# Kernel tuning notes

Hardware: AMD Instinct MI355X
Metric: run time of the kernel (lower is better)

The kernel has to match this reference:

```python
import jax, jax.numpy as jnp
import numpy as np

BS, T, NE, NA, ED = 32, 64, 32, 8, 128
H, A, NH, NACT = 512, 512, 8, 32
HD = A // NH  # 64
SCALE = np.float32(np.sqrt(HD))


def setup_inputs() -> dict:
    key = jax.random.key(0)
    ks = jax.random.split(key, 12)
    inputs = jax.random.normal(ks[0], (BS, T, NE, ED), jnp.float32)
    obs_mask = jax.random.randint(ks[1], (BS, T, NE, NE), 0, 2, jnp.int32)
    scenario_mask = jax.random.randint(ks[2], (BS, T, NE), 0, 2, jnp.int32)
    hidden_state = jnp.zeros((BS * NA, H), jnp.float32)
    g = lambda k, shp: jax.random.normal(k, shp, jnp.float32) * 0.05
    return {
        'inputs': inputs, 'obs_mask': obs_mask, 'scenario_mask': scenario_mask,
        'hidden_state': hidden_state,
        'W1': g(ks[3], (ED, H)), 'b1': jnp.zeros((H,), jnp.float32),
        'Wq': g(ks[4], (H, A)), 'bq': jnp.zeros((A,), jnp.float32),
        'Wk': g(ks[5], (H, A)), 'bk': jnp.zeros((A,), jnp.float32),
        'Wv': g(ks[6], (H, A)), 'bv': jnp.zeros((A,), jnp.float32),
        'Wih': g(ks[7], (3 * H, A)), 'bih': jnp.zeros((3 * H,), jnp.float32),
        'Whh': g(ks[8], (3 * H, H)), 'bhh': jnp.zeros((3 * H,), jnp.float32),
        'Wo': g(ks[9], (H, NACT)), 'bo': jnp.zeros((NACT,), jnp.float32),
    }


def reference(inputs, obs_mask, scenario_mask, hidden_state,
              W1, b1, Wq, bq, Wk, bk, Wv, bv, Wih, bih, Whh, bhh, Wo, bo):
    # fc1: embed every entity  [BS,T,NE,H]
    x = jax.nn.relu(inputs @ W1 + b1)
    q = (x @ Wq + bq).reshape(BS, T, NE, NH, HD)[:, :, :NA]   # agent queries
    k = (x @ Wk + bk).reshape(BS, T, NE, NH, HD)
    v = jax.nn.relu(x @ Wv + bv).reshape(BS, T, NE, NH, HD)
    # scores [BS,T,NH,NA,NE]
    score = jnp.einsum('btqhe,btkhe->bthqk', q, k) / SCALE
    am = obs_mask[:, :, :NA, :].astype(bool)                  # [BS,T,NA,NE]
    score = jnp.where(am[:, :, None], -jnp.inf, score)
    w = jax.nn.softmax(score, axis=-1)
    w = jnp.where(jnp.isnan(w), 0.0, w)                       # fully-masked rows -> 0
    att = jnp.einsum('bthqk,btkhe->btqhe', w, v).reshape(BS, T, NA, A)
    agent_mask = scenario_mask[:, :, :NA].astype(bool)        # [BS,T,NA]
    att = jnp.where(agent_mask[..., None], 0.0, att)
    # per-timestep GRUCell over flattened (BS*NA) rows
    xs = att.transpose(1, 0, 2, 3).reshape(T, BS * NA, A)
    def step(h, xt):
        gi = xt @ Wih.T + bih
        gh = h @ Whh.T + bhh
        ir, iz, inn = jnp.split(gi, 3, axis=-1)
        hr, hz, hn = jnp.split(gh, 3, axis=-1)
        r = jax.nn.sigmoid(ir + hr)
        z = jax.nn.sigmoid(iz + hz)
        n = jnp.tanh(inn + r * hn)
        hn_ = (1.0 - z) * n + z * h
        return hn_, hn_
    _, hs = jax.lax.scan(step, hidden_state, xs)              # [T,BS*NA,H]
    hs = hs.reshape(T, BS, NA, H).transpose(1, 0, 2, 3)       # [BS,T,NA,H]
    qout = hs @ Wo + bo                                       # [BS,T,NA,NACT]
    hs = jnp.where(agent_mask[..., None], 0.0, hs)
    qout = jnp.where(agent_mask[..., None], 0.0, qout)
    return qout, hs
```

## Files before the change

kernel.cpp:

```cpp
#include <hip/hip_runtime.h>
#include <hip/hip_bf16.h>
#include <cstddef>
#include <cstdint>

typedef __hip_bfloat16 bf16;
typedef __attribute__((ext_vector_type(2))) _Float16 half2v;
typedef __attribute__((ext_vector_type(8))) _Float16 half8;
typedef __attribute__((ext_vector_type(8))) short short8;
typedef __attribute__((ext_vector_type(4))) float f32x4;
typedef __attribute__((ext_vector_type(2))) unsigned long long u64x2;

__device__ inline float ldf(const float* p) { return *p; }
__device__ inline float ldf(const bf16* p) { return __bfloat162float(*p); }
__device__ inline void stf(float* p, float v) { *p = v; }
__device__ inline void stf(bf16* p, float v) { *p = __float2bfloat16(v); }
__device__ inline short bfb(float v) { return __builtin_bit_cast(short, __float2bfloat16(v)); }

__device__ inline half8 h8_from(unsigned long long lo, unsigned long long hi) {
    u64x2 t; t.x = lo; t.y = hi;
    return __builtin_bit_cast(half8, t);
}
__device__ inline float fsig(float x) {
    x = fminf(fmaxf(x, -60.f), 60.f);
    return 1.f / (1.f + __expf(-x));
}
__device__ inline float ftanh(float x) {
    x = fminf(fmaxf(x, -15.f), 15.f);
    float e = __expf(2.f * x);
    return 1.f - 2.f / (e + 1.f);
}
__device__ inline void unpack8(uint4 u, float4& lo, float4& hi) {
    uint32_t w0 = u.x, w1 = u.y, w2 = u.z, w3 = u.w;
    lo.x = __builtin_bit_cast(float, (w0 & 0xffffu) << 16);
    lo.y = __builtin_bit_cast(float, w0 & 0xffff0000u);
    lo.z = __builtin_bit_cast(float, (w1 & 0xffffu) << 16);
    lo.w = __builtin_bit_cast(float, w1 & 0xffff0000u);
    hi.x = __builtin_bit_cast(float, (w2 & 0xffffu) << 16);
    hi.y = __builtin_bit_cast(float, w2 & 0xffff0000u);
    hi.z = __builtin_bit_cast(float, (w3 & 0xffffu) << 16);
    hi.w = __builtin_bit_cast(float, w3 & 0xffff0000u);
}


template<int ACT, bool QG, typename TA, typename TC>
__global__ __launch_bounds__(256) void mfma_gemm_k(
    const TA* __restrict__ A, const bf16* __restrict__ Bt,
    const float* __restrict__ bias, TC* __restrict__ C,
    int M, int N, int K)
{
    __shared__ short As[4096];
    __shared__ short Bs[4096];
    const int tid = threadIdx.x;
    const int lane = tid & 63, wid = tid >> 6;
    const int wm = wid >> 1, wn = wid & 1;
    const int bm = blockIdx.y * 128, bn = blockIdx.x * 128;
    const int fr = lane & 15, fq = lane >> 4;

    f32x4 acc[4][4] = {};

    for (int k0 = 0; k0 < K; k0 += 32) {
#if __has_builtin(__builtin_amdgcn_global_load_lds)
        #pragma unroll
        for (int j = 0; j < 2; ++j) {
            int jj = wid * 2 + j;
            int row = jj * 16 + (lane >> 2);
            const short* src = (const short*)Bt + (size_t)(bn + row) * K + k0 + (lane & 3) * 8;
            __builtin_amdgcn_global_load_lds(
                (const __attribute__((address_space(1))) void*)src,
                (__attribute__((address_space(3))) void*)&Bs[jj * 512], 16, 0, 0);
        }
        if constexpr (sizeof(TA) == 2) {
            #pragma unroll
            for (int j = 0; j < 2; ++j) {
                int jj = wid * 2 + j;
                int row = jj * 16 + (lane >> 2);
                int gm = bm + row;
                int ar = QG ? (((gm >> 3) << 5) | (gm & 7)) : gm;
                const short* src = (const short*)A + (size_t)ar * K + k0 + (lane & 3) * 8;
                __builtin_amdgcn_global_load_lds(
                    (const __attribute__((address_space(1))) void*)src,
                    (__attribute__((address_space(3))) void*)&As[jj * 512], 16, 0, 0);
            }
        } else {
            int sr = tid >> 1, sk = (tid & 1) * 16;
            int gm = bm + sr;
            int ar = QG ? (((gm >> 3) << 5) | (gm & 7)) : gm;
            const float* ap = (const float*)A + (size_t)ar * K + k0 + sk;
            float4 f0 = *(const float4*)(ap);
            float4 f1 = *(const float4*)(ap + 4);
            float4 f2 = *(const float4*)(ap + 8);
            float4 f3 = *(const float4*)(ap + 12);
            short tmp[16] = {bfb(f0.x), bfb(f0.y), bfb(f0.z), bfb(f0.w),
                             bfb(f1.x), bfb(f1.y), bfb(f1.z), bfb(f1.w),
                             bfb(f2.x), bfb(f2.y), bfb(f2.z), bfb(f2.w),
                             bfb(f3.x), bfb(f3.y), bfb(f3.z), bfb(f3.w)};
            *(uint4*)&As[sr * 32 + sk]     = *(const uint4*)&tmp[0];
            *(uint4*)&As[sr * 32 + sk + 8] = *(const uint4*)&tmp[8];
        }
#else
        {
            int sr = tid >> 1, sk = (tid & 1) * 16;
            int gm = bm + sr;
            int ar = QG ? (((gm >> 3) << 5) | (gm & 7)) : gm;
            if constexpr (sizeof(TA) == 4) {
                const float* ap = (const float*)A + (size_t)ar * K + k0 + sk;
                short tmp[16];
                #pragma unroll
                for (int j = 0; j < 16; ++j) tmp[j] = bfb(ap[j]);
                *(uint4*)&As[sr * 32 + sk]     = *(const uint4*)&tmp[0];
                *(uint4*)&As[sr * 32 + sk + 8] = *(const uint4*)&tmp[8];
            } else {
                const short* ap = (const short*)A + (size_t)ar * K + k0 + sk;
                *(uint4*)&As[sr * 32 + sk]     = *(const uint4*)(ap);
                *(uint4*)&As[sr * 32 + sk + 8] = *(const uint4*)(ap + 8);
            }
            const short* bp = (const short*)Bt + (size_t)(bn + sr) * K + k0 + sk;
            *(uint4*)&Bs[sr * 32 + sk]     = *(const uint4*)(bp);
            *(uint4*)&Bs[sr * 32 + sk + 8] = *(const uint4*)(bp + 8);
        }
#endif
        __syncthreads();

        short8 af[4], bg[4];
        #pragma unroll
        for (int m = 0; m < 4; ++m)
            af[m] = *(const short8*)&As[(wm * 64 + m * 16 + fr) * 32 + fq * 8];
        #pragma unroll
        for (int n = 0; n < 4; ++n)
            bg[n] = *(const short8*)&Bs[(wn * 64 + n * 16 + fr) * 32 + fq * 8];
        #pragma unroll
        for (int m = 0; m < 4; ++m)
            #pragma unroll
            for (int n = 0; n < 4; ++n)
                acc[m][n] = __builtin_amdgcn_mfma_f32_16x16x32_bf16(
                    af[m], bg[n], acc[m][n], 0, 0, 0);
        __syncthreads();
    }

    #pragma unroll
    for (int m = 0; m < 4; ++m) {
        #pragma unroll
        for (int n = 0; n < 4; ++n) {
            int col = bn + wn * 64 + n * 16 + fr;
            float bv = bias[col];
            #pragma unroll
            for (int r = 0; r < 4; ++r) {
                int row = bm + wm * 64 + m * 16 + fq * 4 + r;
                float v = acc[m][n][r] + bv;
                if (ACT == 1) v = fmaxf(v, 0.f);
                if (ACT == 2 && col >= 512) v = fmaxf(v, 0.f);
                stf(&C[(size_t)row * N + col], v);
            }
        }
    }
}

__global__ __launch_bounds__(256) void prep_all_k(
    const float* __restrict__ W1, const float* __restrict__ Wq,
    const float* __restrict__ Wk, const float* __restrict__ Wv,
    const float* __restrict__ h0,
    const float* __restrict__ bk, const float* __restrict__ bv,
    bf16* __restrict__ W1t, bf16* __restrict__ Wqt, bf16* __restrict__ Wkvt,
    _Float16* __restrict__ ha, float* __restrict__ bkv)
{
    int blk = blockIdx.x;
    int tid = threadIdx.x;
    if (blk < 832) {
        const float* src; bf16* dst; int K, ti;
        if (blk < 64)       { src = W1; dst = W1t;  K = 128; ti = blk; }
        else if (blk < 320) { src = Wq; dst = Wqt;  K = 512; ti = blk - 64; }
        else if (blk < 576) { src = Wk; dst = Wkvt; K = 512; ti = blk - 320; }
        else                { src = Wv; dst = Wkvt + 512 * 512; K = 512; ti = blk - 576; }
        int kt = K >> 5;
        int tk = ti % kt, tn = ti / kt;
        int k0 = tk * 32, n0 = tn * 32;
        __shared__ float tile[32][33];
        int tx = tid & 31, ty = tid >> 5;
        #pragma unroll
        for (int i = 0; i < 4; ++i) {
            int r = ty + i * 8;
            tile[r][tx] = src[(size_t)(k0 + r) * 512 + n0 + tx];
        }
        __syncthreads();
        #pragma unroll
        for (int i = 0; i < 4; ++i) {
            int r = ty + i * 8;
            dst[(size_t)(n0 + r) * K + k0 + tx] = __float2bfloat16(tile[tx][r]);
        }
        return;
    }
    int idx = (blk - 832) * 256 + tid;
    if (idx < 131072) { ha[idx] = (_Float16)h0[idx]; return; }
    idx -= 131072;
    if (idx < 1024) { bkv[idx] = (idx < 512) ? bk[idx] : bv[idx - 512]; return; }
}

template<int ACT, bool BT, bool QG, bool MASKQ, typename TA, typename TB, typename TC>
__global__ __launch_bounds__(256) void gemm_k(
    const TA* __restrict__ A, const TB* __restrict__ B,
    const float* __restrict__ bias, TC* __restrict__ C,
    int M, int N, int K, const int* __restrict__ smask)
{
    const int BM = 64, BN = 64, BK = 16;
    __shared__ float Asl[BM][BK + 1];
    __shared__ float Bsl[BK][BN + 1];
    int tid = threadIdx.x;
    int n0 = blockIdx.x * BN;
    int m0 = blockIdx.y * BM;
    int ty = tid >> 4, tx = tid & 15;
    float acc[4][4] = {};

    for (int k0 = 0; k0 < K; k0 += BK) {
        #pragma unroll
        for (int i = 0; i < 4; ++i) {
            int l = tid * 4 + i;
            int r = l >> 4, c = l & 15;
            int gm = m0 + r;
            int ar = QG ? (((gm >> 3) << 5) | (gm & 7)) : gm;
            Asl[r][c] = ldf(&A[(size_t)ar * K + k0 + c]);
        }
        #pragma unroll
        for (int i = 0; i < 4; ++i) {
            int l = tid * 4 + i;
            if (BT) {
                int n = l >> 4, kk = l & 15;
                int gn = n0 + n;
                Bsl[kk][n] = (gn < N) ? ldf(&B[(size_t)gn * K + k0 + kk]) : 0.f;
            } else {
                int r = l >> 6, c = l & 63;
                int gn = n0 + c;
                Bsl[r][c] = (gn < N) ? ldf(&B[(size_t)(k0 + r) * N + gn]) : 0.f;
            }
        }
        __syncthreads();
        #pragma unroll
        for (int kk = 0; kk < BK; ++kk) {
            float a[4], b[4];
            #pragma unroll
            for (int i = 0; i < 4; ++i) a[i] = Asl[ty + i * 16][kk];
            #pragma unroll
            for (int j = 0; j < 4; ++j) b[j] = Bsl[kk][tx + j * 16];
            #pragma unroll
            for (int i = 0; i < 4; ++i)
                #pragma unroll
                for (int j = 0; j < 4; ++j) acc[i][j] += a[i] * b[j];
        }
        __syncthreads();
    }

    #pragma unroll
    for (int i = 0; i < 4; ++i) {
        int gm = m0 + ty + i * 16;
        bool mz = false;
        if (MASKQ) {
            int a_ = gm & 7, t_ = (gm >> 3) & 63, b_ = gm >> 9;
            mz = smask[((b_ << 6) + t_) * 32 + a_] != 0;
        }
        #pragma unroll
        for (int j = 0; j < 4; ++j) {
            int gn = n0 + tx + j * 16;
            if (gn < N) {
                float v = acc[i][j] + bias[gn];
                if (ACT == 1) v = fmaxf(v, 0.f);
                if (MASKQ && mz) v = 0.f;
                stf(&C[(size_t)gm * N + gn], v);
            }
        }
    }
}

#define AST 68
__global__ __launch_bounds__(64) void attn_k(
    const bf16* __restrict__ qb, const bf16* __restrict__ kb, const bf16* __restrict__ vb,
    const int* __restrict__ obs, const int* __restrict__ smask, bf16* __restrict__ xs,
    int kvstride)
{
    __shared__ float qs[8 * AST], ks[32 * AST], vs[32 * AST], wsm[8 * 32];
    int bid = blockIdx.x;
    int h = bid & 7;
    int bt = bid >> 3;
    int t = bt & 63, b = bt >> 6;
    int tid = threadIdx.x;

    {
        int srow = tid >> 3, c0 = (tid & 7) * 8;
        float4 lo, hi;
        uint4 qv = *(const uint4*)&qb[((size_t)bt * 8 + srow) * 512 + h * 64 + c0];
        unpack8(qv, lo, hi);
        *(float4*)&qs[srow * AST + c0] = lo;
        *(float4*)&qs[srow * AST + c0 + 4] = hi;
        #pragma unroll
        for (int i = 0; i < 4; ++i) {
            int row = srow + i * 8;
            uint4 kv4 = *(const uint4*)&kb[((size_t)bt * 32 + row) * kvstride + h * 64 + c0];
            unpack8(kv4, lo, hi);
            *(float4*)&ks[row * AST + c0] = lo;
            *(float4*)&ks[row * AST + c0 + 4] = hi;
            uint4 vv4 = *(const uint4*)&vb[((size_t)bt * 32 + row) * kvstride + h * 64 + c0];
            unpack8(vv4, lo, hi);
            *(float4*)&vs[row * AST + c0] = lo;
            *(float4*)&vs[row * AST + c0 + 4] = hi;
        }
    }
    __syncthreads();

    int ql = tid >> 3, jl = tid & 7;
    float s[4];
    #pragma unroll
    for (int c = 0; c < 4; ++c) {
        int kl = jl + c * 8;
        float acc = 0.f;
        for (int d = 0; d < 64; ++d) acc += qs[ql * AST + d] * ks[kl * AST + d];
        acc *= 0.125f;
        bool m = obs[(((size_t)bt * 32) + ql) * 32 + kl] != 0;
        s[c] = m ? -__builtin_inff() : acc;
    }
    float mx = fmaxf(fmaxf(s[0], s[1]), fmaxf(s[2], s[3]));
    for (int off = 1; off < 8; off <<= 1) mx = fmaxf(mx, __shfl_xor(mx, off));
    float e4[4]; float sum = 0.f;
    bool allmasked = (mx == -__builtin_inff());
    #pragma unroll
    for (int c = 0; c < 4; ++c) {
        e4[c] = (allmasked || s[c] == -__builtin_inff()) ? 0.f : expf(s[c] - mx);
        sum += e4[c];
    }
    for (int off = 1; off < 8; off <<= 1) sum += __shfl_xor(sum, off);
    float inv = (sum > 0.f) ? 1.f / sum : 0.f;
    #pragma unroll
    for (int c = 0; c < 4; ++c) wsm[ql * 32 + jl + c * 8] = e4[c] * inv;
    __syncthreads();

    bool amask = smask[(size_t)bt * 32 + ql] != 0;
    #pragma unroll
    for (int dd = 0; dd < 8; ++dd) {
        int d = jl + dd * 8;
        float acc = 0.f;
        for (int kl = 0; kl < 32; ++kl) acc += wsm[ql * 32 + kl] * vs[kl * AST + d];
        if (amask) acc = 0.f;
        xs[((size_t)(t * 256 + b * 8 + ql)) * 512 + h * 64 + d] = __float2bfloat16(acc);
    }
}

__global__ __launch_bounds__(128, 1) void gru_xcd_k(
    const bf16* __restrict__ xs, const float* __restrict__ Wih,
    const float* __restrict__ bih,
    const float* __restrict__ Whh, const float* __restrict__ bhh,
    const float* __restrict__ h0,
    const int* __restrict__ smask, float* __restrict__ hs_out,
    _Float16* __restrict__ ha, _Float16* __restrict__ hb, int* __restrict__ flags)
{
    __shared__ _Float16 wh16[48 * 520];
    __shared__ short    wi16[48 * 520];
    const int tid = threadIdx.x;
    const int lane = tid & 63, wid = tid >> 6;
    const int g = blockIdx.x;
    const int grp = g & 7, cu = g >> 3;
    const int r0 = grp * 32;
    const int hc0 = cu * 16;
    const int fr = lane & 15, fq = lane >> 4;
    const int hcol = hc0 + fr;
    const int rw0 = r0 + wid * 16;
    const int row0 = rw0 + fq * 4;

    for (int i = tid; i < 6144; i += 128) {
        int flat = i * 4;
        int r = flat >> 9, c = flat & 511;
        int wr = (r >> 4) * 512 + hc0 + (r & 15);
        float4 v = *(const float4*)(Whh + (size_t)wr * 512 + c);
        half2v p0; p0[0] = (_Float16)v.x; p0[1] = (_Float16)v.y;
        half2v p1; p1[0] = (_Float16)v.z; p1[1] = (_Float16)v.w;
        *(uint32_t*)&wh16[r * 520 + c]     = __builtin_bit_cast(uint32_t, p0);
        *(uint32_t*)&wh16[r * 520 + c + 2] = __builtin_bit_cast(uint32_t, p1);
        float4 u = *(const float4*)(Wih + (size_t)wr * 512 + c);
        uint32_t w0 = (uint32_t)(uint16_t)bfb(u.x) | ((uint32_t)(uint16_t)bfb(u.y) << 16);
        uint32_t w1 = (uint32_t)(uint16_t)bfb(u.z) | ((uint32_t)(uint16_t)bfb(u.w) << 16);
        *(uint32_t*)&wi16[r * 520 + c]     = w0;
        *(uint32_t*)&wi16[r * 520 + c + 2] = w1;
    }

    const float bhr = bhh[hcol], bhz = bhh[512 + hcol], bhn = bhh[1024 + hcol];
    const float bir = bih[hcol], biz = bih[512 + hcol], bin_ = bih[1024 + hcol];

    float hp[4];
    #pragma unroll
    for (int r = 0; r < 4; ++r)
        hp[r] = h0[(size_t)(row0 + r) * 512 + hcol];

    __syncthreads();

    f32x4 gcur[3] = {};
    int mcur[4];
    {
        const short* xp = (const short*)xs + ((size_t)0 * 256 + rw0 + fr) * 512 + fq * 8;
        short8 ax[16];
        #pragma unroll
        for (int ks = 0; ks < 16; ++ks) ax[ks] = *(const short8*)(xp + ks * 32);
        #pragma unroll
        for (int ks = 0; ks < 16; ++ks) {
            const short* bb = &wi16[fr * 520 + ks * 32 + fq * 8];
            short8 b0 = *(const short8*)(bb);
            short8 b1 = *(const short8*)(bb + 16 * 520);
            short8 b2 = *(const short8*)(bb + 32 * 520);
            gcur[0] = __builtin_amdgcn_mfma_f32_16x16x32_bf16(ax[ks], b0, gcur[0], 0, 0, 0);
            gcur[1] = __builtin_amdgcn_mfma_f32_16x16x32_bf16(ax[ks], b1, gcur[1], 0, 0, 0);
            gcur[2] = __builtin_amdgcn_mfma_f32_16x16x32_bf16(ax[ks], b2, gcur[2], 0, 0, 0);
        }
        #pragma unroll
        for (int r = 0; r < 4; ++r) {
            int row = row0 + r;
            mcur[r] = smask[(((row >> 3) << 6) + 0) * 32 + (row & 7)];
        }
    }

    for (int t = 0; t < 64; ++t) {
        const _Float16* hsrc = (t & 1) ? hb : ha;
        _Float16*       hdst = (t & 1) ? ha : hb;

        half8 aA[16];
        {
            const unsigned long long* ap = (const unsigned long long*)
                (hsrc + (size_t)(rw0 + fr) * 512 + fq * 8);
            #pragma unroll
            for (int ks = 0; ks < 16; ++ks) {
                unsigned long long lo = __hip_atomic_load(ap + ks * 8,
                    __ATOMIC_RELAXED, __HIP_MEMORY_SCOPE_AGENT);
                unsigned long long hi = __hip_atomic_load(ap + ks * 8 + 1,
                    __ATOMIC_RELAXED, __HIP_MEMORY_SCOPE_AGENT);
                aA[ks] = h8_from(lo, hi);
            }
        }

        f32x4 acc[3] = {};
        #pragma unroll
        for (int ks = 0; ks < 16; ++ks) {
            const _Float16* bbase = &wh16[fr * 520 + ks * 32 + fq * 8];
            half8 b0 = *(const half8*)(bbase);
            half8 b1 = *(const half8*)(bbase + 16 * 520);
            half8 b2 = *(const half8*)(bbase + 32 * 520);
            acc[0] = __builtin_amdgcn_mfma_f32_16x16x32_f16(aA[ks], b0, acc[0], 0, 0, 0);
            acc[1] = __builtin_amdgcn_mfma_f32_16x16x32_f16(aA[ks], b1, acc[1], 0, 0, 0);
            acc[2] = __builtin_amdgcn_mfma_f32_16x16x32_f16(aA[ks], b2, acc[2], 0, 0, 0);
        }

        float hnv[4];
        #pragma unroll
        for (int r = 0; r < 4; ++r) {
            float rg = fsig(gcur[0][r] + bir + acc[0][r] + bhr);
            float zg = fsig(gcur[1][r] + biz + acc[1][r] + bhz);
            float ng = ftanh(gcur[2][r] + bin_ + rg * (acc[2][r] + bhn));
            float hn = (1.f - zg) * ng + zg * hp[r];
            hp[r] = hn;
            hnv[r] = hn;
            unsigned short hbits = __builtin_bit_cast(unsigned short, (_Float16)hn);
            __hip_atomic_store((unsigned short*)(hdst + (size_t)(row0 + r) * 512 + hcol),
                               hbits, __ATOMIC_RELAXED, __HIP_MEMORY_SCOPE_AGENT);
        }

        if (t != 63) {
            asm volatile("s_waitcnt vmcnt(0)" ::: "memory");
            __builtin_amdgcn_sched_barrier(0);
            if (lane == 0)
                __hip_atomic_store(flags + ((size_t)grp * 64 + t) * 64 + cu * 2 + wid, 1,
                                   __ATOMIC_RELAXED, __HIP_MEMORY_SCOPE_AGENT);
            #pragma unroll
            for (int r = 0; r < 4; ++r) {
                int row = row0 + r;
                int b_ = row >> 3, a_ = row & 7;
                hs_out[((size_t)((b_ << 6) + t) * 8 + a_) * 512 + hcol] =
                    mcur[r] ? 0.f : hnv[r];
            }
            f32x4 gnx[3] = {};
            {
                const short* xp = (const short*)xs +
                    ((size_t)(t + 1) * 256 + rw0 + fr) * 512 + fq * 8;
                short8 ax[16];
                #pragma unroll
                for (int ks = 0; ks < 16; ++ks) ax[ks] = *(const short8*)(xp + ks * 32);
                #pragma unroll
                for (int ks = 0; ks < 16; ++ks) {
                    const short* bb = &wi16[fr * 520 + ks * 32 + fq * 8];
                    short8 b0 = *(const short8*)(bb);
                    short8 b1 = *(const short8*)(bb + 16 * 520);
                    short8 b2 = *(const short8*)(bb + 32 * 520);
                    gnx[0] = __builtin_amdgcn_mfma_f32_16x16x32_bf16(ax[ks], b0, gnx[0], 0, 0, 0);
                    gnx[1] = __builtin_amdgcn_mfma_f32_16x16x32_bf16(ax[ks], b1, gnx[1], 0, 0, 0);
                    gnx[2] = __builtin_amdgcn_mfma_f32_16x16x32_bf16(ax[ks], b2, gnx[2], 0, 0, 0);
                }
            }
            int mnx[4];
            #pragma unroll
            for (int r = 0; r < 4; ++r) {
                int row = row0 + r;
                mnx[r] = smask[(((row >> 3) << 6) + (t + 1)) * 32 + (row & 7)];
            }
            const int* fp = flags + ((size_t)grp * 64 + t) * 64 + lane;
            long it = 0;
            for (;;) {
                int f = __hip_atomic_load(fp, __ATOMIC_RELAXED, __HIP_MEMORY_SCOPE_AGENT);
                if (__all(f != 0) || it > 100000000L) break;
                __builtin_amdgcn_s_sleep(1);
                ++it;
            }
            __builtin_amdgcn_sched_barrier(0);
            gcur[0] = gnx[0]; gcur[1] = gnx[1]; gcur[2] = gnx[2];
            mcur[0] = mnx[0]; mcur[1] = mnx[1]; mcur[2] = mnx[2]; mcur[3] = mnx[3];
        } else {
            #pragma unroll
            for (int r = 0; r < 4; ++r) {
                int row = row0 + r;
                int b_ = row >> 3, a_ = row & 7;
                hs_out[((size_t)((b_ << 6) + t) * 8 + a_) * 512 + hcol] =
                    mcur[r] ? 0.f : hnv[r];
            }
        }
    }
}

extern "C" void kernel_launch(void* const* d_in, const int* in_sizes, int n_in,
                              void* d_out, int out_size, void* d_ws, size_t ws_size,
                              hipStream_t stream)
{
    const float* inputs = (const float*)d_in[0];
    const int*   obs    = (const int*)d_in[1];
    const int*   smask  = (const int*)d_in[2];
    const float* h0     = (const float*)d_in[3];
    const float* W1  = (const float*)d_in[4];  const float* b1  = (const float*)d_in[5];
    const float* Wq  = (const float*)d_in[6];  const float* bq  = (const float*)d_in[7];
    const float* Wk  = (const float*)d_in[8];  const float* bk  = (const float*)d_in[9];
    const float* Wv  = (const float*)d_in[10]; const float* bv  = (const float*)d_in[11];
    const float* Wih = (const float*)d_in[12]; const float* bih = (const float*)d_in[13];
    const float* Whh = (const float*)d_in[14]; const float* bhh = (const float*)d_in[15];
    const float* Wo  = (const float*)d_in[16]; const float* bo  = (const float*)d_in[17];

    char* ws = (char*)d_ws;
    bf16*  x    = (bf16*)(ws + 0);
    bf16*  xs   = (bf16*)(ws + 0);
    bf16*  qb   = (bf16*)(ws + 67108864ull);
    bf16*  kv   = (bf16*)(ws + 83886080ull);
    bf16*  W1t  = (bf16*)(ws + 218103808ull);
    bf16*  Wqt  = (bf16*)(ws + 218234880ull);
    bf16*  Wkvt = (bf16*)(ws + 218759168ull);
    _Float16* ha = (_Float16*)(ws + 219807744ull);
    _Float16* hb = (_Float16*)(ws + 220069888ull);
    int*   flags = (int*)(ws + 220332032ull);
    float* bkv   = (float*)(ws + 220463104ull);

    float* out    = (float*)d_out;
    float* hs_out = out + 524288;

    hipMemsetAsync(flags, 0, 131072, stream);

    prep_all_k<<<dim3(1349), 256, 0, stream>>>(
        W1, Wq, Wk, Wv, h0, bk, bv, W1t, Wqt, Wkvt, ha, bkv);
    mfma_gemm_k<1, false, float, bf16><<<dim3(4, 512), 256, 0, stream>>>(
        inputs, W1t, b1, x, 65536, 512, 128);
    mfma_gemm_k<0, true, bf16, bf16><<<dim3(4, 128), 256, 0, stream>>>(
        x, Wqt, bq, qb, 16384, 512, 512);
    mfma_gemm_k<2, false, bf16, bf16><<<dim3(8, 512), 256, 0, stream>>>(
        x, Wkvt, bkv, kv, 65536, 1024, 512);
    attn_k<<<dim3(16384), 64, 0, stream>>>(qb, kv, kv + 512, obs, smask, xs, 1024);
    gru_xcd_k<<<dim3(256), 128, 0, stream>>>(
        xs, Wih, bih, Whh, bhh, h0, smask, hs_out, ha, hb, flags);
    gemm_k<0, false, false, true><<<dim3(1, 256), 256, 0, stream>>>(
        hs_out, Wo, bo, out, 16384, 32, 512, smask);
}
```

Baseline: 660.9 us.

## Use MFMA for output projection, byte flags and busy-spin in GRU sync

Replaces the scalar fp32 tiled GEMM for the final hs@Wo projection with a bf16 MFMA kernel that reads a pre-transposed bf16 Wo produced in the prep kernel. The GRU cross-block synchronization flags shrink from int to byte, which reduces the memset size and the polling footprint, and the s_sleep in the spin loop is removed to cut wake-up latency. The risks are bf16 rounding of hs in the output projection and higher power or contention from tight spinning.

New measurement: 642.6 us. 1.03x faster.

```diff
diff --git a/kernel.cpp b/kernel.cpp
--- a/kernel.cpp
+++ b/kernel.cpp
@@ -158,19 +158,20 @@
 __global__ __launch_bounds__(256) void prep_all_k(
     const float* __restrict__ W1, const float* __restrict__ Wq,
     const float* __restrict__ Wk, const float* __restrict__ Wv,
-    const float* __restrict__ h0,
+    const float* __restrict__ Wo, const float* __restrict__ h0,
     const float* __restrict__ bk, const float* __restrict__ bv,
     bf16* __restrict__ W1t, bf16* __restrict__ Wqt, bf16* __restrict__ Wkvt,
-    _Float16* __restrict__ ha, float* __restrict__ bkv)
+    bf16* __restrict__ Wot, _Float16* __restrict__ ha, float* __restrict__ bkv)
 {
     int blk = blockIdx.x;
     int tid = threadIdx.x;
-    if (blk < 832) {
-        const float* src; bf16* dst; int K, ti;
-        if (blk < 64)       { src = W1; dst = W1t;  K = 128; ti = blk; }
-        else if (blk < 320) { src = Wq; dst = Wqt;  K = 512; ti = blk - 64; }
-        else if (blk < 576) { src = Wk; dst = Wkvt; K = 512; ti = blk - 320; }
-        else                { src = Wv; dst = Wkvt + 512 * 512; K = 512; ti = blk - 576; }
+    if (blk < 848) {
+        const float* src; bf16* dst; int K, N, ti;
+        if (blk < 64)       { src = W1; dst = W1t;  K = 128; N = 512; ti = blk; }
+        else if (blk < 320) { src = Wq; dst = Wqt;  K = 512; N = 512; ti = blk - 64; }
+        else if (blk < 576) { src = Wk; dst = Wkvt; K = 512; N = 512; ti = blk - 320; }
+        else if (blk < 832) { src = Wv; dst = Wkvt + 512 * 512; K = 512; N = 512; ti = blk - 576; }
+        else                { src = Wo; dst = Wot;  K = 512; N = 32;  ti = blk - 832; }
         int kt = K >> 5;
         int tk = ti % kt, tn = ti / kt;
         int k0 = tk * 32, n0 = tn * 32;
@@ -179,91 +180,85 @@
         #pragma unroll
         for (int i = 0; i < 4; ++i) {
             int r = ty + i * 8;
-            tile[r][tx] = src[(size_t)(k0 + r) * 512 + n0 + tx];
+            tile[r][tx] = src[(size_t)(k0 + r) * N + n0 + tx];
         }
         __syncthreads();
         #pragma unroll
         for (int i = 0; i < 4; ++i) {
             int r = ty + i * 8;
-            dst[(size_t)(n0 + r) * K + k0 + tx] = __float2bfloat16(tile[tx][r]);
+            if (n0 + r < N)
+                dst[(size_t)(n0 + r) * K + k0 + tx] = __float2bfloat16(tile[tx][r]);
         }
         return;
     }
-    int idx = (blk - 832) * 256 + tid;
+    int idx = (blk - 848) * 256 + tid;
     if (idx < 131072) { ha[idx] = (_Float16)h0[idx]; return; }
     idx -= 131072;
     if (idx < 1024) { bkv[idx] = (idx < 512) ? bk[idx] : bv[idx - 512]; return; }
 }
 
-template<int ACT, bool BT, bool QG, bool MASKQ, typename TA, typename TB, typename TC>
-__global__ __launch_bounds__(256) void gemm_k(
-    const TA* __restrict__ A, const TB* __restrict__ B,
-    const float* __restrict__ bias, TC* __restrict__ C,
-    int M, int N, int K, const int* __restrict__ smask)
+__global__ __launch_bounds__(256) void qout_mfma_k(
+    const float* __restrict__ hs, const bf16* __restrict__ Wot,
+    const float* __restrict__ bo, const int* __restrict__ smask,
+    float* __restrict__ out)
 {
-    const int BM = 64, BN = 64, BK = 16;
-    __shared__ float Asl[BM][BK + 1];
-    __shared__ float Bsl[BK][BN + 1];
-    int tid = threadIdx.x;
-    int n0 = blockIdx.x * BN;
-    int m0 = blockIdx.y * BM;
-    int ty = tid >> 4, tx = tid & 15;
-    float acc[4][4] = {};
-
-    for (int k0 = 0; k0 < K; k0 += BK) {
-        #pragma unroll
-        for (int i = 0; i < 4; ++i) {
-            int l = tid * 4 + i;
-            int r = l >> 4, c = l & 15;
-            int gm = m0 + r;
-            int ar = QG ? (((gm >> 3) << 5) | (gm & 7)) : gm;
-            Asl[r][c] = ldf(&A[(size_t)ar * K + k0 + c]);
-        }
-        #pragma unroll
-        for (int i = 0; i < 4; ++i) {
-            int l = tid * 4 + i;
-            if (BT) {
-                int n = l >> 4, kk = l & 15;
-                int gn = n0 + n;
-                Bsl[kk][n] = (gn < N) ? ldf(&B[(size_t)gn * K + k0 + kk]) : 0.f;
-            } else {
-                int r = l >> 6, c = l & 63;
-                int gn = n0 + c;
-                Bsl[r][c] = (gn < N) ? ldf(&B[(size_t)(k0 + r) * N + gn]) : 0.f;
-            }
+    __shared__ short Bs2[32 * 520];
+    __shared__ short As2[128 * 32];
+    const int tid = threadIdx.x;
+    const int lane = tid & 63, wid = tid >> 6;
+    const int bm = blockIdx.x * 128;
+    const int fr = lane & 15, fq = lane >> 4;
+
+    for (int i = tid; i < 2048; i += 256) {
+        int row = i >> 6, col = (i & 63) * 8;
+        *(uint4*)&Bs2[row * 520 + col] = *(const uint4*)((const short*)Wot + row * 512 + col);
+    }
+
+    f32x4 acc[2][2] = {};
+    for (int k0 = 0; k0 < 512; k0 += 32) {
+        {
+            int sr = tid >> 1, sk = (tid & 1) * 16;
+            const float* ap = hs + (size_t)(bm + sr) * 512 + k0 + sk;
+            float4 f0 = *(const float4*)(ap);
+            float4 f1 = *(const float4*)(ap + 4);
+            float4 f2 = *(const float4*)(ap + 8);
+            float4 f3 = *(const float4*)(ap + 12);
+            short tmp[16] = {bfb(f0.x), bfb(f0.y), bfb(f0.z), bfb(f0.w),
+                             bfb(f1.x), bfb(f1.y), bfb(f1.z), bfb(f1.w),
+                             bfb(f2.x), bfb(f2.y), bfb(f2.z), bfb(f2.w),
+                             bfb(f3.x), bfb(f3.y), bfb(f3.z), bfb(f3.w)};
+            *(uint4*)&As2[sr * 32 + sk]     = *(const uint4*)&tmp[0];
+            *(uint4*)&As2[sr * 32 + sk + 8] = *(const uint4*)&tmp[8];
         }
         __syncthreads();
-        #pragma unroll
-        for (int kk = 0; kk < BK; ++kk) {
-            float a[4], b[4];
-            #pragma unroll
-            for (int i = 0; i < 4; ++i) a[i] = Asl[ty + i * 16][kk];
-            #pragma unroll
-            for (int j = 0; j < 4; ++j) b[j] = Bsl[kk][tx + j * 16];
-            #pragma unroll
-            for (int i = 0; i < 4; ++i)
-                #pragma unroll
-                for (int j = 0; j < 4; ++j) acc[i][j] += a[i] * b[j];
-        }
+        short8 af[2], bg[2];
+        #pragma unroll
+        for (int m = 0; m < 2; ++m)
+            af[m] = *(const short8*)&As2[(wid * 32 + m * 16 + fr) * 32 + fq * 8];
+        #pragma unroll
+        for (int n = 0; n < 2; ++n)
+            bg[n] = *(const short8*)&Bs2[(n * 16 + fr) * 520 + k0 + fq * 8];
+        #pragma unroll
+        for (int m = 0; m < 2; ++m)
+            #pragma unroll
+            for (int n = 0; n < 2; ++n)
+                acc[m][n] = __builtin_amdgcn_mfma_f32_16x16x32_bf16(
+                    af[m], bg[n], acc[m][n], 0, 0, 0);
         __syncthreads();
     }
 
     #pragma unroll
-    for (int i = 0; i < 4; ++i) {
-        int gm = m0 + ty + i * 16;
-        bool mz = false;
-        if (MASKQ) {
-            int a_ = gm & 7, t_ = (gm >> 3) & 63, b_ = gm >> 9;
-            mz = smask[((b_ << 6) + t_) * 32 + a_] != 0;
-        }
-        #pragma unroll
-        for (int j = 0; j < 4; ++j) {
-            int gn = n0 + tx + j * 16;
-            if (gn < N) {
-                float v = acc[i][j] + bias[gn];
-                if (ACT == 1) v = fmaxf(v, 0.f);
-                if (MASKQ && mz) v = 0.f;
-                stf(&C[(size_t)gm * N + gn], v);
+    for (int m = 0; m < 2; ++m) {
+        #pragma unroll
+        for (int n = 0; n < 2; ++n) {
+            int col = n * 16 + fr;
+            float bv = bo[col];
+            #pragma unroll
+            for (int r = 0; r < 4; ++r) {
+                int row = bm + wid * 32 + m * 16 + fq * 4 + r;
+                int a_ = row & 7, t_ = (row >> 3) & 63, b_ = row >> 9;
+                bool mz = smask[((b_ << 6) + t_) * 32 + a_] != 0;
+                out[(size_t)row * 32 + col] = mz ? 0.f : (acc[m][n][r] + bv);
             }
         }
     }
@@ -347,7 +342,8 @@
     const float* __restrict__ Whh, const float* __restrict__ bhh,
     const float* __restrict__ h0,
     const int* __restrict__ smask, float* __restrict__ hs_out,
-    _Float16* __restrict__ ha, _Float16* __restrict__ hb, int* __restrict__ flags)
+    _Float16* __restrict__ ha, _Float16* __restrict__ hb,
+    unsigned char* __restrict__ flags8)
 {
     __shared__ _Float16 wh16[48 * 520];
     __shared__ short    wi16[48 * 520];
@@ -460,7 +456,8 @@
             asm volatile("s_waitcnt vmcnt(0)" ::: "memory");
             __builtin_amdgcn_sched_barrier(0);
             if (lane == 0)
-                __hip_atomic_store(flags + ((size_t)grp * 64 + t) * 64 + cu * 2 + wid, 1,
+                __hip_atomic_store(flags8 + ((size_t)grp * 64 + t) * 64 + cu * 2 + wid,
+                                   (unsigned char)1,
                                    __ATOMIC_RELAXED, __HIP_MEMORY_SCOPE_AGENT);
             #pragma unroll
             for (int r = 0; r < 4; ++r) {
@@ -493,12 +490,12 @@
                 int row = row0 + r;
                 mnx[r] = smask[(((row >> 3) << 6) + (t + 1)) * 32 + (row & 7)];
             }
-            const int* fp = flags + ((size_t)grp * 64 + t) * 64 + lane;
+            const unsigned char* fp = flags8 + ((size_t)grp * 64 + t) * 64 + lane;
             long it = 0;
             for (;;) {
-                int f = __hip_atomic_load(fp, __ATOMIC_RELAXED, __HIP_MEMORY_SCOPE_AGENT);
-                if (__all(f != 0) || it > 100000000L) break;
-                __builtin_amdgcn_s_sleep(1);
+                unsigned char f = __hip_atomic_load(fp, __ATOMIC_RELAXED,
+                                                    __HIP_MEMORY_SCOPE_AGENT);
+                if (__all(f != 0) || it > 200000000L) break;
                 ++it;
             }
             __builtin_amdgcn_sched_barrier(0);
@@ -542,16 +539,17 @@
     bf16*  Wkvt = (bf16*)(ws + 218759168ull);
     _Float16* ha = (_Float16*)(ws + 219807744ull);
     _Float16* hb = (_Float16*)(ws + 220069888ull);
-    int*   flags = (int*)(ws + 220332032ull);
-    float* bkv   = (float*)(ws + 220463104ull);
+    unsigned char* flags8 = (unsigned char*)(ws + 220332032ull);
+    float* bkv  = (float*)(ws + 220364800ull);
+    bf16*  Wot  = (bf16*)(ws + 220368896ull);
 
     float* out    = (float*)d_out;
     float* hs_out = out + 524288;
 
-    hipMemsetAsync(flags, 0, 131072, stream);
-
-    prep_all_k<<<dim3(1349), 256, 0, stream>>>(
-        W1, Wq, Wk, Wv, h0, bk, bv, W1t, Wqt, Wkvt, ha, bkv);
+    hipMemsetAsync(flags8, 0, 32768, stream);
+
+    prep_all_k<<<dim3(1365), 256, 0, stream>>>(
+        W1, Wq, Wk, Wv, Wo, h0, bk, bv, W1t, Wqt, Wkvt, Wot, ha, bkv);
     mfma_gemm_k<1, false, float, bf16><<<dim3(4, 512), 256, 0, stream>>>(
         inputs, W1t, b1, x, 65536, 512, 128);
     mfma_gemm_k<0, true, bf16, bf16><<<dim3(4, 128), 256, 0, stream>>>(
@@ -560,7 +558,6 @@
         x, Wkvt, bkv, kv, 65536, 1024, 512);
     attn_k<<<dim3(16384), 64, 0, stream>>>(qb, kv, kv + 512, obs, smask, xs, 1024);
     gru_xcd_k<<<dim3(256), 128, 0, stream>>>(
-        xs, Wih, bih, Whh, bhh, h0, smask, hs_out, ha, hb, flags);
-    gemm_k<0, false, false, true><<<dim3(1, 256), 256, 0, stream>>>(
-        hs_out, Wo, bo, out, 16384, 32, 512, smask);
-}
+        xs, Wih, bih, Whh, bhh, h0, smask, hs_out, ha, hb, flags8);
+    qout_mfma_k<<<dim3(128), 256, 0, stream>>>(hs_out, Wot, bo, smask, out);
+}
```
